# Kernel tuning notes

Hardware: AMD Instinct MI355X
Metric: run time of the kernel (lower is better)

Reference implementation:

```python
import jax, jax.numpy as jnp
import numpy as np

B, N, OBS = 512, 64, 256
H1, H2 = 4, 4
D = 128            # embed/key dim (d_k_1 = d_k_2 = 128)
O1 = D // H1       # 32, per-head value dim stage 1
O2 = D // H2       # 32, per-head value dim stage 2
IN2 = O1 * H1      # 128, input dim to stage 2
FOUT = 16          # final_output_dim


def setup_inputs() -> dict:
    key = jax.random.key(0)
    ks = jax.random.split(key, 22)
    g = lambda k, shp: (jax.random.normal(k, shp, dtype=jnp.float32) * 0.05)
    inp = {
        "states": jax.random.normal(ks[0], (B, N, OBS), dtype=jnp.float32),
        # stage 1 per-head params, stacked over heads
        "E1_w": g(ks[1], (H1, D, OBS)), "E1_b": g(ks[2], (H1, D)),
        "K1_w": g(ks[3], (H1, D, D)),   "K1_b": g(ks[4], (H1, D)),
        "Q1_w": g(ks[5], (H1, D, D)),   "Q1_b": g(ks[6], (H1, D)),
        "V1_w": g(ks[7], (H1, O1, D)),  "V1_b": g(ks[8], (H1, O1)),
        # stage 2 per-head params
        "E2_w": g(ks[9], (H2, D, IN2)), "E2_b": g(ks[10], (H2, D)),
        "K2_w": g(ks[11], (H2, D, D)),  "K2_b": g(ks[12], (H2, D)),
        "Q2_w": g(ks[13], (H2, D, D)),  "Q2_b": g(ks[14], (H2, D)),
        "V2_w": g(ks[15], (H2, O2, D)), "V2_b": g(ks[16], (H2, O2)),
        # final MLP policy head
        "F1_w": g(ks[17], (64, O2 * H2)), "F1_b": g(ks[18], (64,)),
        "F2_w": g(ks[19], (FOUT, 64)),    "F2_b": g(ks[20], (FOUT,)),
    }
    return inp


def _attn_block(x, Ew, Eb, Kw, Kb, Qw, Qb, Vw, Vb, d_k):
    # x: [B,N,I]; all head loops batched via leading head axis h
    se = jax.nn.leaky_relu(jnp.einsum('bni,hdi->hbnd', x, Ew) + Eb[:, None, None, :])  # [h,B,N,D]
    k = jnp.einsum('hbnd,hed->hbne', se, Kw) + Kb[:, None, None, :]
    q = jnp.einsum('hbnd,hed->hbne', se, Qw) + Qb[:, None, None, :]
    w = jax.nn.softmax(jnp.einsum('hbne,hbme->hbnm', q, k) / jnp.sqrt(jnp.float32(d_k)), axis=-1)  # [h,B,N,N]
    v = jax.nn.leaky_relu(jnp.einsum('hbnd,hod->hbno', se, Vw) + Vb[:, None, None, :])  # [h,B,N,O]
    att = jnp.einsum('hbnm,hbmo->hbno', w, v)
    h, b, n, o = att.shape
    return jnp.transpose(att, (1, 2, 0, 3)).reshape(b, n, h * o), w


def reference(states, E1_w, E1_b, K1_w, K1_b, Q1_w, Q1_b, V1_w, V1_b,
              E2_w, E2_b, K2_w, K2_b, Q2_w, Q2_b, V2_w, V2_b,
              F1_w, F1_b, F2_w, F2_b):
    x1, w1 = _attn_block(states, E1_w, E1_b, K1_w, K1_b, Q1_w, Q1_b, V1_w, V1_b, D)
    x2, w2 = _attn_block(x1, E2_w, E2_b, K2_w, K2_b, Q2_w, Q2_b, V2_w, V2_b, D)
    h = jax.nn.leaky_relu(jnp.einsum('bnf,of->bno', x2, F1_w) + F1_b)
    policy = jax.nn.softmax(jnp.einsum('bno,po->bnp', h, F2_w) + F2_b, axis=-1)
    return policy, w1, w2
```

## Files before the change

### kernel.cpp

```cpp
#include <hip/hip_runtime.h>

typedef __attribute__((ext_vector_type(8))) short short8;
typedef __attribute__((ext_vector_type(4))) float f32x4;
typedef __attribute__((ext_vector_type(2))) unsigned uint2v;

#define MFMA(a, b, c) __builtin_amdgcn_mfma_f32_16x16x32_bf16((a), (b), (c), 0, 0, 0)

__device__ __forceinline__ short f2bf(float f) {
    union { float f; unsigned u; } v; v.f = f;
    unsigned r = v.u + 0x7fffu + ((v.u >> 16) & 1u);
    return (short)(r >> 16);
}
__device__ __forceinline__ float bf2f(short s) {
    union { unsigned u; float f; } v; v.u = ((unsigned)(unsigned short)s) << 16; return v.f;
}
__device__ __forceinline__ unsigned pkbf(float lo, float hi) {
    return (unsigned)(unsigned short)f2bf(lo) | ((unsigned)(unsigned short)f2bf(hi) << 16);
}
__device__ __forceinline__ float lrelu(float v) { return (v >= 0.f) ? v : 0.01f * v; }

__device__ __forceinline__ void load_lds16(const void* g, void* l) {
    __builtin_amdgcn_global_load_lds((const __attribute__((address_space(1))) void*)g,
                                     (__attribute__((address_space(3))) void*)l, 16, 0, 0);
}

struct ConvArgs { const float* src[7]; int end[7]; };

__global__ __launch_bounds__(256) void convert_weights_kernel(ConvArgs a,
                                                              short* __restrict__ dstw,
                                                              short* __restrict__ dstx) {
    int i4 = blockIdx.x * 256 + threadIdx.x;
    int seg = 0;
#pragma unroll
    for (int s = 0; s < 6; s++) seg += (i4 >= a.end[s]) ? 1 : 0;
    int base = (seg == 0) ? 0 : a.end[seg - 1];
    float4 v = ((const float4*)a.src[seg])[i4 - base];
    uint2v o = { pkbf(v.x, v.y), pkbf(v.z, v.w) };
    short* dst = (seg == 6) ? (dstx + (size_t)(i4 - a.end[5]) * 4)
                            : (dstw + (size_t)i4 * 4);
    *(uint2v*)dst = o;
}

__global__ __launch_bounds__(256) void precompute_gt_kernel(
    const float* __restrict__ Q1w, const float* __restrict__ K1w, const float* __restrict__ Q1b,
    const float* __restrict__ Q2w, const float* __restrict__ K2w, const float* __restrict__ Q2b,
    short* __restrict__ gt, float* __restrict__ wvec) {
    const int s  = blockIdx.x >> 8;
    const int h  = (blockIdx.x >> 6) & 3;
    const int fg = blockIdx.x & 63;
    const float* Qw = (s ? Q2w : Q1w) + (size_t)h * 16384;
    const float* Kw = (s ? K2w : K1w) + (size_t)h * 16384;
    const float* qb = (s ? Q2b : Q1b) + h * 128;
    const int f = fg * 2 + (threadIdx.x >> 7);
    const int e = threadIdx.x & 127;
    float acc = 0.f, accw = 0.f;
#pragma unroll 8
    for (int c = 0; c < 128; c++) {
        float kv = Kw[c * 128 + f];
        acc  = fmaf(Qw[c * 128 + e], kv, acc);
        accw = fmaf(qb[c], kv, accw);
    }
    const float scale = 0.08838834764831845f;
    gt[((size_t)((s * 4 + h) * 128 + f)) * 128 + e] = f2bf(acc * scale);
    if (e == 0) wvec[(s * 4 + h) * 128 + f] = accw * scale;
}

template<int IN>
__global__ __launch_bounds__(256, (IN == 256) ? 3 : 4) void attn_stage_kernel(
    const short* __restrict__ xin,
    const short* __restrict__ Ew, const float* __restrict__ Eb,
    const short* __restrict__ Gt, const float* __restrict__ wvec,
    const short* __restrict__ Vw, const float* __restrict__ Vb,
    float* __restrict__ w_out,
    short* __restrict__ x_out)
{
    constexpr int OFF_T  = 0;
    constexpr int OFF_SE = 64 * IN;
    constexpr int OFF_VT = (IN == 256) ? 8192 : (64 * IN + 8704);
    constexpr int OFF_CB = OFF_VT + 2304;
    constexpr int SMEM   = (IN == 256) ? 25088 : 19328;
    __shared__ short sm[SMEM];

    const int tid  = threadIdx.x;
    const int b    = blockIdx.x & 511;
    const int h    = blockIdx.x >> 9;
    const int wv   = tid >> 6;
    const int lane = tid & 63;
    const int quad = lane >> 4;
    const int l16  = lane & 15;
    const int myrow = wv * 16 + l16;
    constexpr int NK1 = IN / 32;

    {
        const short* xg = xin + (size_t)b * 64 * IN;
#pragma unroll
        for (int t = 0; t < IN / 32; t++) {
            int off   = wv * 16 * IN + t * 512 + lane * 8;
            int row   = off / IN;
            int chunk = (off % IN) >> 3;
            int src   = row * IN + ((chunk ^ (row & 7)) << 3);
            load_lds16(xg + src, &sm[wv * 16 * IN + t * 512]);
        }
    }

    short8 ebf[NK1 * 2];
    {
        const short* ewh = Ew + (size_t)h * 128 * IN;
#pragma unroll
        for (int k0i = 0; k0i < NK1; k0i++)
#pragma unroll
            for (int j = 0; j < 2; j++)
                ebf[k0i * 2 + j] = *(const short8*)(ewh + (size_t)(wv * 32 + j * 16 + l16) * IN + k0i * 32 + quad * 8);
    }
    __syncthreads();

    short8 gtf[8];

    {
        f32x4 acc[4][2];
#pragma unroll
        for (int j = 0; j < 2; j++) {
            f32x4 eb4 = *(const f32x4*)&Eb[h * 128 + wv * 32 + j * 16 + quad * 4];
#pragma unroll
            for (int i = 0; i < 4; i++) acc[i][j] = eb4;
        }
        __builtin_amdgcn_s_setprio(1);
#pragma unroll
        for (int k0i = 0; k0i < NK1; k0i++) {
            short8 x8[4];
#pragma unroll
            for (int i = 0; i < 4; i++) {
                int xrow = i * 16 + l16;
                int kc = k0i * 4 + quad;
                x8[i] = *(const short8*)&sm[xrow * IN + ((kc ^ (xrow & 7)) << 3)];
            }
#pragma unroll
            for (int i = 0; i < 4; i++)
#pragma unroll
                for (int j = 0; j < 2; j++)
                    acc[i][j] = MFMA(ebf[k0i * 2 + j], x8[i], acc[i][j]);
        }
        __builtin_amdgcn_s_setprio(0);
        {
            const short* gth = Gt + (size_t)h * 16384;
#pragma unroll
            for (int k0i = 0; k0i < 4; k0i++)
#pragma unroll
                for (int j = 0; j < 2; j++)
                    gtf[k0i * 2 + j] = *(const short8*)(gth + (size_t)(wv * 32 + j * 16 + l16) * 128 + k0i * 32 + quad * 8);
        }
#pragma unroll
        for (int i = 0; i < 4; i++)
#pragma unroll
            for (int j = 0; j < 2; j++) {
                uint2v o = { pkbf(lrelu(acc[i][j][0]), lrelu(acc[i][j][1])),
                             pkbf(lrelu(acc[i][j][2]), lrelu(acc[i][j][3])) };
                *(uint2v*)&sm[OFF_SE + (i * 16 + l16) * 136 + wv * 32 + j * 16 + quad * 4] = o;
            }
    }
    __syncthreads();

    {
        f32x4 tacc[4][2];
        f32x4 z = {0.f, 0.f, 0.f, 0.f};
#pragma unroll
        for (int i = 0; i < 4; i++)
#pragma unroll
            for (int j = 0; j < 2; j++) tacc[i][j] = z;
        __builtin_amdgcn_s_setprio(1);
#pragma unroll
        for (int k0i = 0; k0i < 4; k0i++) {
            short8 se8[4];
#pragma unroll
            for (int i = 0; i < 4; i++)
                se8[i] = *(const short8*)&sm[OFF_SE + (i * 16 + l16) * 136 + k0i * 32 + quad * 8];
#pragma unroll
            for (int i = 0; i < 4; i++)
#pragma unroll
                for (int j = 0; j < 2; j++)
                    tacc[i][j] = MFMA(gtf[k0i * 2 + j], se8[i], tacc[i][j]);
        }
#pragma unroll
        for (int i = 0; i < 4; i++)
#pragma unroll
            for (int j = 0; j < 2; j++) {
                uint2v ot = { pkbf(tacc[i][j][0], tacc[i][j][1]),
                              pkbf(tacc[i][j][2], tacc[i][j][3]) };
                int trow = i * 16 + l16;
                int c = wv * 4 + j * 2 + (quad >> 1);
                *(uint2v*)&sm[OFF_T + trow * 128 + ((c ^ (trow & 7)) << 3) + (quad & 1) * 4] = ot;
            }

        const short* vwh = Vw + (size_t)h * 32 * 128;
        const int n0v = (wv >> 1) * 16, mrow = (wv & 1) * 32;
        short8 vbf[4];
#pragma unroll
        for (int k0i = 0; k0i < 4; k0i++)
            vbf[k0i] = *(const short8*)(vwh + (size_t)(n0v + l16) * 128 + k0i * 32 + quad * 8);
        float vb = Vb[h * 32 + n0v + l16];
        f32x4 vacc[2];
        vacc[0] = (f32x4){vb, vb, vb, vb}; vacc[1] = vacc[0];
#pragma unroll
        for (int k0i = 0; k0i < 4; k0i++) {
            short8 a0 = *(const short8*)&sm[OFF_SE + (mrow + l16) * 136 + k0i * 32 + quad * 8];
            short8 a1 = *(const short8*)&sm[OFF_SE + (mrow + 16 + l16) * 136 + k0i * 32 + quad * 8];
            vacc[0] = MFMA(a0, vbf[k0i], vacc[0]);
            vacc[1] = MFMA(a1, vbf[k0i], vacc[1]);
        }
        __builtin_amdgcn_s_setprio(0);
#pragma unroll
        for (int i = 0; i < 2; i++) {
            uint2v ov = { pkbf(lrelu(vacc[i][0]), lrelu(vacc[i][1])),
                          pkbf(lrelu(vacc[i][2]), lrelu(vacc[i][3])) };
            *(uint2v*)&sm[OFF_VT + (n0v + l16) * 72 + mrow + i * 16 + quad * 4] = ov;
        }

        {
            const float* wvh = wvec + h * 128;
            const int row = wv * 16 + (lane >> 2);
            const int e0 = (lane & 3) * 32;
            float s = 0.f;
#pragma unroll
            for (int u = 0; u < 32; u += 8) {
                short8 sv = *(const short8*)&sm[OFF_SE + row * 136 + e0 + u];
                float4 w0 = *(const float4*)(wvh + e0 + u);
                float4 w1 = *(const float4*)(wvh + e0 + u + 4);
                s = fmaf(bf2f(sv[0]), w0.x, s); s = fmaf(bf2f(sv[1]), w0.y, s);
                s = fmaf(bf2f(sv[2]), w0.z, s); s = fmaf(bf2f(sv[3]), w0.w, s);
                s = fmaf(bf2f(sv[4]), w1.x, s); s = fmaf(bf2f(sv[5]), w1.y, s);
                s = fmaf(bf2f(sv[6]), w1.z, s); s = fmaf(bf2f(sv[7]), w1.w, s);
            }
            s += __shfl_xor(s, 1, 4);
            s += __shfl_xor(s, 2, 4);
            if ((lane & 3) == 0) ((float*)&sm[OFF_CB])[row] = s;
        }
    }
    __syncthreads();

    f32x4 lacc[4];
#pragma unroll
    for (int jj = 0; jj < 4; jj++) lacc[jj] = (f32x4){0.f, 0.f, 0.f, 0.f};
    __builtin_amdgcn_s_setprio(1);
#pragma unroll
    for (int k0 = 0; k0 < 128; k0 += 32) {
        int kc = (k0 >> 3) + quad;
        short8 tf = *(const short8*)&sm[OFF_T + myrow * 128 + ((kc ^ (myrow & 7)) << 3)];
#pragma unroll
        for (int jj = 0; jj < 4; jj++) {
            short8 af = *(const short8*)&sm[OFF_SE + (jj * 16 + l16) * 136 + k0 + quad * 8];
            lacc[jj] = MFMA(af, tf, lacc[jj]);
        }
    }
    __builtin_amdgcn_s_setprio(0);

    {
        const float* cbf = (const float*)&sm[OFF_CB];
#pragma unroll
        for (int jj = 0; jj < 4; jj++) {
            f32x4 cb4 = *(const f32x4*)&cbf[jj * 16 + quad * 4];
            lacc[jj] += cb4;
        }
        float m01 = fmaxf(fmaxf(lacc[0][0], lacc[0][1]), fmaxf(lacc[0][2], lacc[0][3]));
        float m23 = fmaxf(fmaxf(lacc[1][0], lacc[1][1]), fmaxf(lacc[1][2], lacc[1][3]));
        float m45 = fmaxf(fmaxf(lacc[2][0], lacc[2][1]), fmaxf(lacc[2][2], lacc[2][3]));
        float m67 = fmaxf(fmaxf(lacc[3][0], lacc[3][1]), fmaxf(lacc[3][2], lacc[3][3]));
        float m = fmaxf(fmaxf(m01, m23), fmaxf(m45, m67));
        m = fmaxf(m, __shfl_xor(m, 16, 64));
        m = fmaxf(m, __shfl_xor(m, 32, 64));
        float sum = 0.f;
#pragma unroll
        for (int jj = 0; jj < 4; jj++)
#pragma unroll
            for (int r = 0; r < 4; r++) {
                float e = __expf(lacc[jj][r] - m);
                lacc[jj][r] = e; sum += e;
            }
        sum += __shfl_xor(sum, 16, 64);
        sum += __shfl_xor(sum, 32, 64);
        float inv = 1.0f / sum;
        float* wbase = w_out + ((size_t)(h * 512 + b)) * 4096 + (size_t)myrow * 64;
#pragma unroll
        for (int jj = 0; jj < 4; jj++) {
            f32x4 w4 = { lacc[jj][0] * inv, lacc[jj][1] * inv, lacc[jj][2] * inv, lacc[jj][3] * inv };
            uint2v o = { pkbf(w4[0], w4[1]), pkbf(w4[2], w4[3]) };
            int c = jj * 2 + (quad >> 1);
            *(uint2v*)&sm[OFF_T + myrow * 128 + ((c ^ (myrow & 7)) << 3) + (quad & 1) * 4] = o;
            __builtin_nontemporal_store(w4, (f32x4*)(wbase + jj * 16 + quad * 4));
        }
    }

    {
        f32x4 aacc[2]; aacc[0] = (f32x4){0.f, 0.f, 0.f, 0.f}; aacc[1] = aacc[0];
#pragma unroll
        for (int k0 = 0; k0 < 64; k0 += 32) {
            int kc = (k0 >> 3) + quad;
            short8 wf = *(const short8*)&sm[OFF_T + myrow * 128 + ((kc ^ (myrow & 7)) << 3)];
#pragma unroll
            for (int o = 0; o < 2; o++) {
                short8 vf = *(const short8*)&sm[OFF_VT + (o * 16 + l16) * 72 + k0 + quad * 8];
                aacc[o] = MFMA(vf, wf, aacc[o]);
            }
        }
        short* xob = x_out + (size_t)b * 8192 + (size_t)myrow * 128 + h * 32;
#pragma unroll
        for (int o = 0; o < 2; o++) {
            uint2v o8 = { pkbf(aacc[o][0], aacc[o][1]), pkbf(aacc[o][2], aacc[o][3]) };
            *(uint2v*)&xob[o * 16 + quad * 4] = o8;
        }
    }
}

#define H_LD 72
__global__ __launch_bounds__(256)
void final_mlp_mfma_kernel(const short* __restrict__ x2,
                           const short* __restrict__ F1wb,
                           const float* __restrict__ F1b,
                           const short* __restrict__ F2wb,
                           const float* __restrict__ F2b,
                           float* __restrict__ policy)
{
    __shared__ short hsm[4][16 * H_LD];
    const int tid  = threadIdx.x;
    const int wv   = tid >> 6;
    const int lane = tid & 63;
    const int quad = lane >> 4;
    const int l16  = lane & 15;
    const int rowbase = blockIdx.x * 64 + wv * 16;

    short8 a[4];
    const short* xrow = x2 + (size_t)(rowbase + l16) * 128;
#pragma unroll
    for (int k = 0; k < 4; k++) a[k] = *(const short8*)(xrow + k * 32 + quad * 8);
    f32x4 acc[4];
#pragma unroll
    for (int j = 0; j < 4; j++) acc[j] = *(const f32x4*)&F1b[j * 16 + quad * 4];
#pragma unroll
    for (int k = 0; k < 4; k++)
#pragma unroll
        for (int j = 0; j < 4; j++) {
            short8 b8 = *(const short8*)(F1wb + (size_t)(j * 16 + l16) * 128 + k * 32 + quad * 8);
            acc[j] = MFMA(b8, a[k], acc[j]);
        }
    short* hh = &hsm[wv][0];
#pragma unroll
    for (int j = 0; j < 4; j++) {
        uint2v o = { pkbf(lrelu(acc[j][0]), lrelu(acc[j][1])),
                     pkbf(lrelu(acc[j][2]), lrelu(acc[j][3])) };
        *(uint2v*)&hh[l16 * H_LD + j * 16 + quad * 4] = o;
    }
    __syncthreads();

    f32x4 lg = *(const f32x4*)&F2b[quad * 4];
#pragma unroll
    for (int k = 0; k < 2; k++) {
        short8 a2 = *(const short8*)(hh + l16 * H_LD + k * 32 + quad * 8);
        short8 b2 = *(const short8*)(F2wb + (size_t)l16 * 64 + k * 32 + quad * 8);
        lg = MFMA(b2, a2, lg);
    }
    float m = fmaxf(fmaxf(lg[0], lg[1]), fmaxf(lg[2], lg[3]));
    m = fmaxf(m, __shfl_xor(m, 16, 64));
    m = fmaxf(m, __shfl_xor(m, 32, 64));
    f32x4 e;
    float s = 0.f;
#pragma unroll
    for (int r = 0; r < 4; r++) { e[r] = __expf(lg[r] - m); s += e[r]; }
    s += __shfl_xor(s, 16, 64);
    s += __shfl_xor(s, 32, 64);
    float inv = 1.0f / s;
    f32x4 p4 = { e[0] * inv, e[1] * inv, e[2] * inv, e[3] * inv };
    __builtin_nontemporal_store(p4, (f32x4*)&policy[(size_t)(rowbase + l16) * 16 + quad * 4]);
}

extern "C" void kernel_launch(void* const* d_in, const int* in_sizes, int n_in,
                              void* d_out, int out_size, void* d_ws, size_t ws_size,
                              hipStream_t stream) {
    const float* states = (const float*)d_in[0];
    const float* E1w = (const float*)d_in[1];  const float* E1b = (const float*)d_in[2];
    const float* K1w = (const float*)d_in[3];  const float* K1b = (const float*)d_in[4];
    const float* Q1w = (const float*)d_in[5];  const float* Q1b = (const float*)d_in[6];
    const float* V1w = (const float*)d_in[7];  const float* V1b = (const float*)d_in[8];
    const float* E2w = (const float*)d_in[9];  const float* E2b = (const float*)d_in[10];
    const float* K2w = (const float*)d_in[11]; const float* K2b = (const float*)d_in[12];
    const float* Q2w = (const float*)d_in[13]; const float* Q2b = (const float*)d_in[14];
    const float* V2w = (const float*)d_in[15]; const float* V2b = (const float*)d_in[16];
    const float* F1w = (const float*)d_in[17]; const float* F1b = (const float*)d_in[18];
    const float* F2w = (const float*)d_in[19]; const float* F2b = (const float*)d_in[20];
    (void)K1b; (void)K2b;

    float* out    = (float*)d_out;
    float* policy = out;
    float* w1     = out + 512 * 64 * 16;
    float* w2     = w1 + 4 * 512 * 64 * 64;

    short* wsb = (short*)d_ws;
    short* x1b = wsb;
    short* xsb = wsb + 4194304;
    short* x2b = xsb;
    short* wts = wsb + 12582912;
    short* wE1 = wts;
    short* wV1 = wts + 131072;
    short* wE2 = wts + 147456;
    short* wV2 = wts + 212992;
    short* wF1 = wts + 229376;
    short* wF2 = wts + 237568;
    short* gt  = wts + 238592;
    float* wvec = (float*)(wts + 238592 + 131072);

    ConvArgs ca;
    ca.src[0] = E1w; ca.src[1] = V1w; ca.src[2] = E2w; ca.src[3] = V2w;
    ca.src[4] = F1w; ca.src[5] = F2w; ca.src[6] = states;
    ca.end[0] = 32768;  ca.end[1] = 36864;  ca.end[2] = 53248;  ca.end[3] = 57344;
    ca.end[4] = 59392;  ca.end[5] = 59648;  ca.end[6] = 2156800;
    convert_weights_kernel<<<8425, 256, 0, stream>>>(ca, wts, xsb);
    precompute_gt_kernel<<<512, 256, 0, stream>>>(Q1w, K1w, Q1b, Q2w, K2w, Q2b, gt, wvec);

    attn_stage_kernel<256><<<2048, 256, 0, stream>>>(
        xsb, wE1, E1b, gt, wvec, wV1, V1b, w1, x1b);
    attn_stage_kernel<128><<<2048, 256, 0, stream>>>(
        x1b, wE2, E2b, gt + 65536, wvec + 512, wV2, V2b, w2, x2b);
    final_mlp_mfma_kernel<<<512, 256, 0, stream>>>(x2b, wF1, F1b, wF2, F2b, policy);
}
```

Measured before the change: 226.4 us.

## Process two heads per attention block sharing input tile; fuse prep kernels

Each attention block now runs 512 threads covering two heads of the same batch element, so the input tile is loaded into LDS once and shared by both heads. This halves the redundant input staging and the grid size. The query-bias term is folded into the T accumulator's initial value, which drops the separate per-row dot-product and its LDS buffer. The weight conversion and G-matrix precompute kernels are merged into a single launch. In exchange, each block uses more LDS and has larger blocks, which can change occupancy.

```diff
diff --git a/kernel.cpp b/kernel.cpp
--- a/kernel.cpp
+++ b/kernel.cpp
@@ -26,47 +26,50 @@
 
 struct ConvArgs { const float* src[7]; int end[7]; };
 
-__global__ __launch_bounds__(256) void convert_weights_kernel(ConvArgs a,
-                                                              short* __restrict__ dstw,
-                                                              short* __restrict__ dstx) {
-    int i4 = blockIdx.x * 256 + threadIdx.x;
-    int seg = 0;
-#pragma unroll
-    for (int s = 0; s < 6; s++) seg += (i4 >= a.end[s]) ? 1 : 0;
-    int base = (seg == 0) ? 0 : a.end[seg - 1];
-    float4 v = ((const float4*)a.src[seg])[i4 - base];
-    uint2v o = { pkbf(v.x, v.y), pkbf(v.z, v.w) };
-    short* dst = (seg == 6) ? (dstx + (size_t)(i4 - a.end[5]) * 4)
-                            : (dstw + (size_t)i4 * 4);
-    *(uint2v*)dst = o;
-}
-
-__global__ __launch_bounds__(256) void precompute_gt_kernel(
-    const float* __restrict__ Q1w, const float* __restrict__ K1w, const float* __restrict__ Q1b,
-    const float* __restrict__ Q2w, const float* __restrict__ K2w, const float* __restrict__ Q2b,
-    short* __restrict__ gt, float* __restrict__ wvec) {
-    const int s  = blockIdx.x >> 8;
-    const int h  = (blockIdx.x >> 6) & 3;
-    const int fg = blockIdx.x & 63;
-    const float* Qw = (s ? Q2w : Q1w) + (size_t)h * 16384;
-    const float* Kw = (s ? K2w : K1w) + (size_t)h * 16384;
-    const float* qb = (s ? Q2b : Q1b) + h * 128;
-    const int f = fg * 2 + (threadIdx.x >> 7);
-    const int e = threadIdx.x & 127;
-    float acc = 0.f, accw = 0.f;
+__global__ __launch_bounds__(256) void conv_and_gt_kernel(ConvArgs a,
+                                                          short* __restrict__ dstw,
+                                                          short* __restrict__ dstx,
+                                                          const float* __restrict__ Q1w, const float* __restrict__ K1w,
+                                                          const float* __restrict__ Q1b,
+                                                          const float* __restrict__ Q2w, const float* __restrict__ K2w,
+                                                          const float* __restrict__ Q2b,
+                                                          short* __restrict__ gt, float* __restrict__ wvec) {
+    if (blockIdx.x < 8425) {
+        int i4 = blockIdx.x * 256 + threadIdx.x;
+        int seg = 0;
+#pragma unroll
+        for (int s = 0; s < 6; s++) seg += (i4 >= a.end[s]) ? 1 : 0;
+        int base = (seg == 0) ? 0 : a.end[seg - 1];
+        float4 v = ((const float4*)a.src[seg])[i4 - base];
+        uint2v o = { pkbf(v.x, v.y), pkbf(v.z, v.w) };
+        short* dst = (seg == 6) ? (dstx + (size_t)(i4 - a.end[5]) * 4)
+                                : (dstw + (size_t)i4 * 4);
+        *(uint2v*)dst = o;
+    } else {
+        int bid = blockIdx.x - 8425;
+        const int s  = bid >> 8;
+        const int h  = (bid >> 6) & 3;
+        const int fg = bid & 63;
+        const float* Qw = (s ? Q2w : Q1w) + (size_t)h * 16384;
+        const float* Kw = (s ? K2w : K1w) + (size_t)h * 16384;
+        const float* qb = (s ? Q2b : Q1b) + h * 128;
+        const int f = fg * 2 + (threadIdx.x >> 7);
+        const int e = threadIdx.x & 127;
+        float acc = 0.f, accw = 0.f;
 #pragma unroll 8
-    for (int c = 0; c < 128; c++) {
-        float kv = Kw[c * 128 + f];
-        acc  = fmaf(Qw[c * 128 + e], kv, acc);
-        accw = fmaf(qb[c], kv, accw);
-    }
-    const float scale = 0.08838834764831845f;
-    gt[((size_t)((s * 4 + h) * 128 + f)) * 128 + e] = f2bf(acc * scale);
-    if (e == 0) wvec[(s * 4 + h) * 128 + f] = accw * scale;
+        for (int c = 0; c < 128; c++) {
+            float kv = Kw[c * 128 + f];
+            acc  = fmaf(Qw[c * 128 + e], kv, acc);
+            accw = fmaf(qb[c], kv, accw);
+        }
+        const float scale = 0.08838834764831845f;
+        gt[((size_t)((s * 4 + h) * 128 + f)) * 128 + e] = f2bf(acc * scale);
+        if (e == 0) wvec[(s * 4 + h) * 128 + f] = accw * scale;
+    }
 }
 
 template<int IN>
-__global__ __launch_bounds__(256, (IN == 256) ? 3 : 4) void attn_stage_kernel(
+__global__ __launch_bounds__(512, 4) void attn_stage_kernel(
     const short* __restrict__ xin,
     const short* __restrict__ Ew, const float* __restrict__ Eb,
     const short* __restrict__ Gt, const float* __restrict__ wvec,
@@ -74,32 +77,34 @@
     float* __restrict__ w_out,
     short* __restrict__ x_out)
 {
-    constexpr int OFF_T  = 0;
-    constexpr int OFF_SE = 64 * IN;
-    constexpr int OFF_VT = (IN == 256) ? 8192 : (64 * IN + 8704);
-    constexpr int OFF_CB = OFF_VT + 2304;
-    constexpr int SMEM   = (IN == 256) ? 25088 : 19328;
-    __shared__ short sm[SMEM];
+    __shared__ short sm[38400];
 
     const int tid  = threadIdx.x;
     const int b    = blockIdx.x & 511;
-    const int h    = blockIdx.x >> 9;
-    const int wv   = tid >> 6;
+    const int h0   = (blockIdx.x >> 9) << 1;
+    const int wv8  = tid >> 6;
+    const int hsel = wv8 >> 2;
+    const int wvl  = wv8 & 3;
+    const int h    = h0 + hsel;
     const int lane = tid & 63;
     const int quad = lane >> 4;
     const int l16  = lane & 15;
-    const int myrow = wv * 16 + l16;
+    const int myrow = wvl * 16 + l16;
+    const int OFF_T  = hsel * 8192;
+    const int OFF_SE = 16384 + hsel * 8704;
+    const int OFF_VT = 33792 + hsel * 2304;
     constexpr int NK1 = IN / 32;
 
     {
         const short* xg = xin + (size_t)b * 64 * IN;
 #pragma unroll
-        for (int t = 0; t < IN / 32; t++) {
-            int off   = wv * 16 * IN + t * 512 + lane * 8;
+        for (int t = 0; t < IN / 64; t++) {
+            int base  = wv8 * 8 * IN + t * 512;
+            int off   = base + lane * 8;
             int row   = off / IN;
             int chunk = (off % IN) >> 3;
             int src   = row * IN + ((chunk ^ (row & 7)) << 3);
-            load_lds16(xg + src, &sm[wv * 16 * IN + t * 512]);
+            load_lds16(xg + src, &sm[base]);
         }
     }
 
@@ -110,7 +115,7 @@
         for (int k0i = 0; k0i < NK1; k0i++)
 #pragma unroll
             for (int j = 0; j < 2; j++)
-                ebf[k0i * 2 + j] = *(const short8*)(ewh + (size_t)(wv * 32 + j * 16 + l16) * IN + k0i * 32 + quad * 8);
+                ebf[k0i * 2 + j] = *(const short8*)(ewh + (size_t)(wvl * 32 + j * 16 + l16) * IN + k0i * 32 + quad * 8);
     }
     __syncthreads();
 
@@ -120,7 +125,7 @@
         f32x4 acc[4][2];
 #pragma unroll
         for (int j = 0; j < 2; j++) {
-            f32x4 eb4 = *(const f32x4*)&Eb[h * 128 + wv * 32 + j * 16 + quad * 4];
+            f32x4 eb4 = *(const f32x4*)&Eb[h * 128 + wvl * 32 + j * 16 + quad * 4];
 #pragma unroll
             for (int i = 0; i < 4; i++) acc[i][j] = eb4;
         }
@@ -147,7 +152,7 @@
             for (int k0i = 0; k0i < 4; k0i++)
 #pragma unroll
                 for (int j = 0; j < 2; j++)
-                    gtf[k0i * 2 + j] = *(const short8*)(gth + (size_t)(wv * 32 + j * 16 + l16) * 128 + k0i * 32 + quad * 8);
+                    gtf[k0i * 2 + j] = *(const short8*)(gth + (size_t)(wvl * 32 + j * 16 + l16) * 128 + k0i * 32 + quad * 8);
         }
 #pragma unroll
         for (int i = 0; i < 4; i++)
@@ -155,18 +160,19 @@
             for (int j = 0; j < 2; j++) {
                 uint2v o = { pkbf(lrelu(acc[i][j][0]), lrelu(acc[i][j][1])),
                              pkbf(lrelu(acc[i][j][2]), lrelu(acc[i][j][3])) };
-                *(uint2v*)&sm[OFF_SE + (i * 16 + l16) * 136 + wv * 32 + j * 16 + quad * 4] = o;
+                *(uint2v*)&sm[OFF_SE + (i * 16 + l16) * 136 + wvl * 32 + j * 16 + quad * 4] = o;
             }
     }
     __syncthreads();
 
     {
         f32x4 tacc[4][2];
-        f32x4 z = {0.f, 0.f, 0.f, 0.f};
-#pragma unroll
-        for (int i = 0; i < 4; i++)
-#pragma unroll
-            for (int j = 0; j < 2; j++) tacc[i][j] = z;
+#pragma unroll
+        for (int j = 0; j < 2; j++) {
+            f32x4 wv4 = *(const f32x4*)&wvec[h * 128 + wvl * 32 + j * 16 + quad * 4];
+#pragma unroll
+            for (int i = 0; i < 4; i++) tacc[i][j] = wv4;
+        }
         __builtin_amdgcn_s_setprio(1);
 #pragma unroll
         for (int k0i = 0; k0i < 4; k0i++) {
@@ -187,12 +193,12 @@
                 uint2v ot = { pkbf(tacc[i][j][0], tacc[i][j][1]),
                               pkbf(tacc[i][j][2], tacc[i][j][3]) };
                 int trow = i * 16 + l16;
-                int c = wv * 4 + j * 2 + (quad >> 1);
+                int c = wvl * 4 + j * 2 + (quad >> 1);
                 *(uint2v*)&sm[OFF_T + trow * 128 + ((c ^ (trow & 7)) << 3) + (quad & 1) * 4] = ot;
             }
 
         const short* vwh = Vw + (size_t)h * 32 * 128;
-        const int n0v = (wv >> 1) * 16, mrow = (wv & 1) * 32;
+        const int n0v = (wvl >> 1) * 16, mrow = (wvl & 1) * 32;
         short8 vbf[4];
 #pragma unroll
         for (int k0i = 0; k0i < 4; k0i++)
@@ -214,26 +220,6 @@
                           pkbf(lrelu(vacc[i][2]), lrelu(vacc[i][3])) };
             *(uint2v*)&sm[OFF_VT + (n0v + l16) * 72 + mrow + i * 16 + quad * 4] = ov;
         }
-
-        {
-            const float* wvh = wvec + h * 128;
-            const int row = wv * 16 + (lane >> 2);
-            const int e0 = (lane & 3) * 32;
-            float s = 0.f;
-#pragma unroll
-            for (int u = 0; u < 32; u += 8) {
-                short8 sv = *(const short8*)&sm[OFF_SE + row * 136 + e0 + u];
-                float4 w0 = *(const float4*)(wvh + e0 + u);
-                float4 w1 = *(const float4*)(wvh + e0 + u + 4);
-                s = fmaf(bf2f(sv[0]), w0.x, s); s = fmaf(bf2f(sv[1]), w0.y, s);
-                s = fmaf(bf2f(sv[2]), w0.z, s); s = fmaf(bf2f(sv[3]), w0.w, s);
-                s = fmaf(bf2f(sv[4]), w1.x, s); s = fmaf(bf2f(sv[5]), w1.y, s);
-                s = fmaf(bf2f(sv[6]), w1.z, s); s = fmaf(bf2f(sv[7]), w1.w, s);
-            }
-            s += __shfl_xor(s, 1, 4);
-            s += __shfl_xor(s, 2, 4);
-            if ((lane & 3) == 0) ((float*)&sm[OFF_CB])[row] = s;
-        }
     }
     __syncthreads();
 
@@ -254,12 +240,6 @@
     __builtin_amdgcn_s_setprio(0);
 
     {
-        const float* cbf = (const float*)&sm[OFF_CB];
-#pragma unroll
-        for (int jj = 0; jj < 4; jj++) {
-            f32x4 cb4 = *(const f32x4*)&cbf[jj * 16 + quad * 4];
-            lacc[jj] += cb4;
-        }
         float m01 = fmaxf(fmaxf(lacc[0][0], lacc[0][1]), fmaxf(lacc[0][2], lacc[0][3]));
         float m23 = fmaxf(fmaxf(lacc[1][0], lacc[1][1]), fmaxf(lacc[1][2], lacc[1][3]));
         float m45 = fmaxf(fmaxf(lacc[2][0], lacc[2][1]), fmaxf(lacc[2][2], lacc[2][3]));
@@ -411,12 +391,12 @@
     ca.src[4] = F1w; ca.src[5] = F2w; ca.src[6] = states;
     ca.end[0] = 32768;  ca.end[1] = 36864;  ca.end[2] = 53248;  ca.end[3] = 57344;
     ca.end[4] = 59392;  ca.end[5] = 59648;  ca.end[6] = 2156800;
-    convert_weights_kernel<<<8425, 256, 0, stream>>>(ca, wts, xsb);
-    precompute_gt_kernel<<<512, 256, 0, stream>>>(Q1w, K1w, Q1b, Q2w, K2w, Q2b, gt, wvec);
-
-    attn_stage_kernel<256><<<2048, 256, 0, stream>>>(
+    conv_and_gt_kernel<<<8937, 256, 0, stream>>>(ca, wts, xsb,
+                                                 Q1w, K1w, Q1b, Q2w, K2w, Q2b, gt, wvec);
+
+    attn_stage_kernel<256><<<1024, 512, 0, stream>>>(
         xsb, wE1, E1b, gt, wvec, wV1, V1b, w1, x1b);
-    attn_stage_kernel<128><<<2048, 256, 0, stream>>>(
+    attn_stage_kernel<128><<<1024, 512, 0, stream>>>(
         x1b, wE2, E2b, gt + 65536, wvec + 512, wV2, V2b, w2, x2b);
     final_mlp_mfma_kernel<<<512, 256, 0, stream>>>(x2b, wF1, F1b, wF2, F2b, policy);
 }
```

New measurement: 217.9 us. -3.8%, faster.
